# Kernel optimization log

Hardware: AMD Instinct MI355X
Metric: run time of the kernel (lower is better)

The kernel has to match this reference:

```python
import jax, jax.numpy as jnp
import numpy as np

N = 50257      # num nodes / vocab
E = 1_608_224  # num edges (~32 avg degree)
D = 64         # static_feat_dim == embed_dim
OUT = 50257    # output classes
M = 2048       # nodes in batch (node_ids)


def setup_inputs() -> dict:
    key = jax.random.key(0)
    ks = jax.random.split(key, 16)
    w = lambda k, s: jax.random.normal(k, s, jnp.float32) * 0.05
    return dict(
        x=jax.random.normal(ks[0], (N, D), jnp.float32),
        src=jax.random.randint(ks[1], (E,), 0, N, jnp.int32),
        dst=jax.random.randint(ks[2], (E,), 0, N, jnp.int32),
        node_ids=jax.random.randint(ks[3], (M,), 0, N, jnp.int32),
        # GCNConv weights for the three GRU gates
        Wz=w(ks[4], (D, D)), bz=jnp.zeros((D,), jnp.float32),
        Wr=w(ks[5], (D, D)), br=jnp.zeros((D,), jnp.float32),
        Wh=w(ks[6], (D, D)), bh=jnp.zeros((D,), jnp.float32),
        # Linear(2D -> D) gate mixers
        Lz=w(ks[7], (2 * D, D)), lbz=jnp.zeros((D,), jnp.float32),
        Lr=w(ks[8], (2 * D, D)), lbr=jnp.zeros((D,), jnp.float32),
        Lh=w(ks[9], (2 * D, D)), lbh=jnp.zeros((D,), jnp.float32),
        # NodePredictor MLP
        W1=w(ks[10], (D, D)), b1=jnp.zeros((D,), jnp.float32),
        W2=w(ks[11], (D, OUT)), b2=jnp.zeros((OUT,), jnp.float32),
    )


def _gcn(x, src, dst, W, b, enorm, snorm):
    """GCNConv with self-loops: out = D^-1/2 (A+I) D^-1/2 (x W) + b."""
    xw = x @ W  # [N, D]
    agg = jnp.zeros_like(xw).at[dst].add(xw[src] * enorm[:, None])
    return agg + xw * snorm[:, None] + b


def reference(x, src, dst, node_ids, Wz, bz, Wr, br, Wh, bh,
              Lz, lbz, Lr, lbr, Lh, lbh, W1, b1, W2, b2):
    n = x.shape[0]
    # degree with self-loops, symmetric normalization
    deg = jnp.zeros((n,), x.dtype).at[dst].add(jnp.ones((), x.dtype)) + 1.0
    dinv = jax.lax.rsqrt(deg)
    enorm = dinv[src] * dinv[dst]   # per-edge norm
    snorm = dinv * dinv             # self-loop norm

    H = jnp.zeros((n, Wz.shape[1]), x.dtype)  # TGCN initial hidden state
    Z = jax.nn.sigmoid(
        jnp.concatenate([_gcn(x, src, dst, Wz, bz, enorm, snorm), H], 1) @ Lz + lbz)
    R = jax.nn.sigmoid(
        jnp.concatenate([_gcn(x, src, dst, Wr, br, enorm, snorm), H], 1) @ Lr + lbr)
    Ht = jnp.tanh(
        jnp.concatenate([_gcn(x, src, dst, Wh, bh, enorm, snorm), H * R], 1) @ Lh + lbh)
    H = Z * H + (1.0 - Z) * Ht  # [N, D]

    zn = H[node_ids]                          # gather batch nodes [M, D]
    h = jax.nn.relu(zn @ W1 + b1)             # NodePredictor hidden
    return h @ W2 + b2                        # logits [M, OUT]
```

## Files before the change

### kernel.cpp

```cpp
#include <hip/hip_runtime.h>

#define DD 64
#define HBLK 128
#define CAP 128

typedef __attribute__((ext_vector_type(8))) __bf16 bf16x8;
typedef __attribute__((ext_vector_type(4))) float f32x4;
typedef __attribute__((ext_vector_type(4), aligned(4))) float f32x4a;
typedef unsigned short u16;
typedef unsigned int u32;

__device__ __forceinline__ u16 f2bf(float f) {
  union { float f; u32 u; } v; v.f = f;
  u32 r = v.u + 0x7FFFu + ((v.u >> 16) & 1u);
  return (u16)(r >> 16);
}


__global__ __launch_bounds__(256) void k_prep(
    const int* __restrict__ dst, const int* __restrict__ ids,
    const float* __restrict__ Wz, const float* __restrict__ bz,
    const float* __restrict__ Wh, const float* __restrict__ bh,
    const float* __restrict__ Lz, const float* __restrict__ lbz,
    const float* __restrict__ Lh, const float* __restrict__ lbh,
    const float* __restrict__ W2, const float* __restrict__ b2,
    u32* __restrict__ partial, int* __restrict__ slot, int* __restrict__ pcnt,
    float* __restrict__ Wzl, float* __restrict__ bzl,
    float* __restrict__ Whl, float* __restrict__ bhl,
    u16* __restrict__ W2t, float* __restrict__ b2p,
    int E, int N, int M, int OUTC, int NPAD, int NB4) {
  extern __shared__ u32 lds[];
  const int tid = threadIdx.x, bid = blockIdx.x;

  if (bid < HBLK) {
    for (int i = tid; i < NB4; i += 256) lds[i] = 0;
    __syncthreads();
    for (int e = bid * 256 + tid; e < E; e += HBLK * 256) {
      int d = dst[e];
      atomicAdd(&lds[d >> 2], 1u << ((d & 3) * 8));
    }
    __syncthreads();
    u32* po = partial + (size_t)bid * NB4;
    for (int i = tid; i < NB4; i += 256) po[i] = lds[i];
  } else if (bid == 128) {
    for (int i = tid; i < N; i += 256) slot[i] = 0;
    __syncthreads();
    for (int i = tid; i < M; i += 256) slot[ids[i]] = i + 1;
    for (int i = tid; i < M; i += 256) pcnt[i] = 0;
  } else if (bid == 129 || bid == 130) {
    const float* W = (bid == 129) ? Wz : Wh;
    const float* bb = (bid == 129) ? bz : bh;
    const float* L = (bid == 129) ? Lz : Lh;
    const float* lb = (bid == 129) ? lbz : lbh;
    float* Wo = (bid == 129) ? Wzl : Whl;
    float* bo = (bid == 129) ? bzl : bhl;
    for (int idx = tid; idx < DD * DD; idx += 256) {
      int i = idx >> 6, j = idx & 63;
      float acc = 0.f;
      for (int k = 0; k < DD; ++k) acc += W[i * DD + k] * L[k * DD + j];
      Wo[idx] = acc;
    }
    if (tid < DD) {
      float acc = lb[tid];
      for (int k = 0; k < DD; ++k) acc += bb[k] * L[k * DD + tid];
      bo[tid] = acc;
    }
  } else if (bid < 139) {
    int part = bid - 131;
    int chunk = (NPAD + 7) / 8;
    int lo = part * chunk, hi = min(lo + chunk, NPAD);
    for (int i = lo + tid; i < hi; i += 256) b2p[i] = (i < OUTC) ? b2[i] : 0.f;
  } else {
    u16* tile = (u16*)lds;
    const int NT = NPAD / DD;
    for (int tl = bid - 139; tl < NT; tl += 117) {
      int o0 = tl * DD;
      __syncthreads();
#pragma unroll
      for (int i = 0; i < 16; ++i) {
        int idx = i * 256 + tid;
        int k = idx >> 6, o = idx & 63;
        int oc = o0 + o;
        float v = (oc < OUTC) ? W2[(size_t)k * OUTC + oc] : 0.f;
        tile[o * 66 + k] = f2bf(v);
      }
      __syncthreads();
#pragma unroll
      for (int i = 0; i < 16; ++i) {
        int idx = i * 256 + tid;
        int o = idx >> 6, k = idx & 63;
        W2t[(size_t)(o0 + o) * DD + k] = tile[o * 66 + k];
      }
    }
  }
}


__global__ __launch_bounds__(256) void k_mid(
    const u32* __restrict__ partial, const int* __restrict__ slot,
    const int* __restrict__ src, const int* __restrict__ dst,
    float* __restrict__ dinv, int* __restrict__ pcnt, int* __restrict__ esrc,
    int E, int N, int NB4) {
  int gid = blockIdx.x * 256 + threadIdx.x;
  if (gid < N) {
    int word = gid >> 2, sh = (gid & 3) * 8;
    u32 s = 0;
    for (int p = 0; p < HBLK; ++p) s += (partial[(size_t)p * NB4 + word] >> sh) & 0xFFu;
    dinv[gid] = rsqrtf(1.f + (float)s);
  }
  if (gid < E) {
    int d = dst[gid];
    int s = slot[d];
    if (s) {
      int j = s - 1;
      int p = atomicAdd(&pcnt[j], 1);
      if (p < CAP) esrc[j * CAP + p] = src[gid];
    }
  }
}


__global__ __launch_bounds__(256) void k_hidden(
    const int* __restrict__ ids, const int* __restrict__ slot,
    const float* __restrict__ x, const float* __restrict__ dinv,
    const int* __restrict__ pcnt, const int* __restrict__ esrc,
    const float* __restrict__ Wzl, const float* __restrict__ bzl,
    const float* __restrict__ Whl, const float* __restrict__ bhl,
    const float* __restrict__ W1, const float* __restrict__ b1,
    u16* __restrict__ hB, int M) {
  __shared__ float sWz[DD * DD], sWh[DD * DD], sW1[DD * DD];
  for (int i = threadIdx.x; i < DD * DD; i += 256) {
    sWz[i] = Wzl[i]; sWh[i] = Whl[i]; sW1[i] = W1[i];
  }
  __syncthreads();
  int wv = threadIdx.x >> 6, t = threadIdx.x & 63;
  int i = blockIdx.x * 4 + wv;
  if (i >= M) return;
  int n = ids[i];
  int j = slot[n] - 1;
  int c = min(pcnt[j], CAP);
  const int4* el4 = (const int4*)(esrc + j * CAP);
  float agg = 0.f;
  int k = 0;
  for (; k + 8 <= c; k += 8) {
    int4 a = el4[k >> 2], b = el4[(k >> 2) + 1];
    agg += x[(size_t)a.x * DD + t] * dinv[a.x] + x[(size_t)a.y * DD + t] * dinv[a.y]
         + x[(size_t)a.z * DD + t] * dinv[a.z] + x[(size_t)a.w * DD + t] * dinv[a.w]
         + x[(size_t)b.x * DD + t] * dinv[b.x] + x[(size_t)b.y * DD + t] * dinv[b.y]
         + x[(size_t)b.z * DD + t] * dinv[b.z] + x[(size_t)b.w * DD + t] * dinv[b.w];
  }
  for (; k + 4 <= c; k += 4) {
    int4 a = el4[k >> 2];
    agg += x[(size_t)a.x * DD + t] * dinv[a.x] + x[(size_t)a.y * DD + t] * dinv[a.y]
         + x[(size_t)a.z * DD + t] * dinv[a.z] + x[(size_t)a.w * DD + t] * dinv[a.w];
  }
  const int* el = esrc + j * CAP;
  for (; k < c; ++k) { int s0 = el[k]; agg += x[(size_t)s0 * DD + t] * dinv[s0]; }
  float di = dinv[n];
  float av = agg * di + x[(size_t)n * DD + t] * di * di;
  float z = bzl[t], h = bhl[t];
#pragma unroll 8
  for (int q = 0; q < DD; ++q) {
    float a = __shfl(av, q);
    z += a * sWz[q * DD + t];
    h += a * sWh[q * DD + t];
  }
  float Z = 1.f / (1.f + expf(-z));
  float Ht = tanhf(h);
  float hv = (1.f - Z) * Ht;
  float oacc = b1[t];
#pragma unroll 8
  for (int q = 0; q < DD; ++q) oacc += __shfl(hv, q) * sW1[q * DD + t];
  hB[(size_t)i * DD + t] = f2bf(fmaxf(oacc, 0.f));
}


__global__ __launch_bounds__(256) void k_gemm(const u16* __restrict__ hB, const u16* __restrict__ W2t,
                                              const float* __restrict__ b2p, float* __restrict__ out,
                                              int OUTC) {
  __shared__ float sOut[64][260];
  int lane = threadIdx.x & 63;
  int wave = threadIdx.x >> 6;
  int l15 = lane & 15;
  int g = (lane >> 4) & 3;
  long cbase = (long)blockIdx.x * 256;
  int rl = wave * 16 + l15;

  for (int rb = 0; rb < 8; ++rb) {
    int row = blockIdx.y * 512 + rb * 64 + rl;
    const bf16x8* hrow = (const bf16x8*)(hB + (size_t)row * DD);
    bf16x8 b0 = hrow[g], b1 = hrow[4 + g];

#pragma unroll
    for (int half = 0; half < 2; ++half) {
      long c0 = cbase + half * 128;
      f32x4 acc[8];
#pragma unroll
      for (int s = 0; s < 8; ++s) {
        long wcol = c0 + s * 16 + l15;
        const bf16x8* wr = (const bf16x8*)(W2t + (size_t)wcol * DD);
        bf16x8 a0 = wr[g], a1 = wr[4 + g];
        f32x4 a = {0.f, 0.f, 0.f, 0.f};
        a = __builtin_amdgcn_mfma_f32_16x16x32_bf16(a0, b0, a, 0, 0, 0);
        a = __builtin_amdgcn_mfma_f32_16x16x32_bf16(a1, b1, a, 0, 0, 0);
        acc[s] = a;
      }
#pragma unroll
      for (int s = 0; s < 8; ++s) {
        int cl = half * 128 + s * 16 + g * 4;
        float4 bias = *(const float4*)(b2p + cbase + cl);
        sOut[rl][cl + 0] = acc[s][0] + bias.x;
        sOut[rl][cl + 1] = acc[s][1] + bias.y;
        sOut[rl][cl + 2] = acc[s][2] + bias.z;
        sOut[rl][cl + 3] = acc[s][3] + bias.w;
      }
    }
#pragma unroll
    for (int rr = 0; rr < 16; ++rr) {
      int lr = wave * 16 + rr;
      long grow = blockIdx.y * 512 + rb * 64 + lr;
      long col = cbase + lane * 4;
      f32x4a v;
      v[0] = sOut[lr][lane * 4 + 0];
      v[1] = sOut[lr][lane * 4 + 1];
      v[2] = sOut[lr][lane * 4 + 2];
      v[3] = sOut[lr][lane * 4 + 3];
      float* p = out + (size_t)grow * OUTC + col;
      if (col + 3 < OUTC) {
        *(f32x4a*)p = v;
      } else {
#pragma unroll
        for (int r = 0; r < 4; ++r) if (col + r < OUTC) p[r] = v[r];
      }
    }
  }
}


extern "C" void kernel_launch(void* const* d_in, const int* in_sizes, int n_in,
                              void* d_out, int out_size, void* d_ws, size_t ws_size,
                              hipStream_t stream) {
  const float* x   = (const float*)d_in[0];
  const int*   src = (const int*)d_in[1];
  const int*   dst = (const int*)d_in[2];
  const int*   ids = (const int*)d_in[3];
  const float* Wz  = (const float*)d_in[4];
  const float* bz  = (const float*)d_in[5];
  const float* Wh  = (const float*)d_in[8];
  const float* bh  = (const float*)d_in[9];
  const float* Lz  = (const float*)d_in[10];
  const float* lbz = (const float*)d_in[11];
  const float* Lh  = (const float*)d_in[14];
  const float* lbh = (const float*)d_in[15];
  const float* W1  = (const float*)d_in[16];
  const float* b1  = (const float*)d_in[17];
  const float* W2  = (const float*)d_in[18];
  const float* b2  = (const float*)d_in[19];

  const int N    = in_sizes[0] / DD;
  const int E    = in_sizes[1];
  const int M    = in_sizes[3];
  const int OUTC = in_sizes[19];
  const int NPAD = (OUTC + 255) & ~255;
  const int NB4  = (N + 3) / 4;

  char* w = (char*)d_ws;
  auto carve = [&](size_t bytes) {
    void* p = (void*)w;
    w += (bytes + 255) & ~(size_t)255;
    return p;
  };
  u32*   partial = (u32*)carve((size_t)HBLK * NB4 * 4);
  float* dinv = (float*)carve((size_t)N * 4);
  int*   slot = (int*)carve((size_t)N * 4);
  int*   pcnt = (int*)carve((size_t)M * 4);
  int*   esrc = (int*)carve((size_t)M * CAP * 4);
  float* Wzl  = (float*)carve(DD * DD * 4);
  float* bzl  = (float*)carve(DD * 4);
  float* Whl  = (float*)carve(DD * DD * 4);
  float* bhl  = (float*)carve(DD * 4);
  u16*   hB   = (u16*)carve((size_t)M * DD * 2);
  u16*   W2t  = (u16*)carve((size_t)NPAD * DD * 2);
  float* b2p  = (float*)carve((size_t)NPAD * 4);

  unsigned shmem = (unsigned)(NB4 * 4);
  hipLaunchKernelGGL(k_prep, dim3(256), dim3(256), shmem, stream,
                     dst, ids, Wz, bz, Wh, bh, Lz, lbz, Lh, lbh, W2, b2,
                     partial, slot, pcnt, Wzl, bzl, Whl, bhl, W2t, b2p,
                     E, N, M, OUTC, NPAD, NB4);
  hipLaunchKernelGGL(k_mid, dim3((E + 255) / 256), dim3(256), 0, stream,
                     partial, slot, src, dst, dinv, pcnt, esrc, E, N, NB4);
  hipLaunchKernelGGL(k_hidden, dim3((M + 3) / 4), dim3(256), 0, stream,
                     ids, slot, x, dinv, pcnt, esrc, Wzl, bzl, Whl, bhl, W1, b1, hB, M);
  hipLaunchKernelGGL(k_gemm, dim3(NPAD / 256, M / 512), dim3(256), 0, stream,
                     hB, W2t, b2p, (float*)d_out, OUTC);
}
```

Baseline: 208.0 us.

## Rebalance work: persistent GEMM scheduling, wider histogram, vectorized transpose and degree reduce

The output GEMM becomes a fixed 512-block persistent kernel. Each block walks a contiguous range of (column-tile, 64-row) units, which evens out load and keeps the same W2t tile in cache across consecutive units. The degree histogram uses twice as many blocks (256), and k_prep's grid grows to 400 so more blocks share the W2 transpose. The transpose itself now uses float4 loads and packed 32-bit stores. k_mid reduces a whole packed word per thread and writes four dinv values at once, though it now has to read twice as many partial histograms.

```diff
diff --git a/kernel.cpp b/kernel.cpp
--- a/kernel.cpp
+++ b/kernel.cpp
@@ -1,8 +1,9 @@
 #include <hip/hip_runtime.h>
 
 #define DD 64
-#define HBLK 128
+#define HB2 256
 #define CAP 128
+#define GBLK 512
 
 typedef __attribute__((ext_vector_type(8))) __bf16 bf16x8;
 typedef __attribute__((ext_vector_type(4))) float f32x4;
@@ -32,28 +33,28 @@
   extern __shared__ u32 lds[];
   const int tid = threadIdx.x, bid = blockIdx.x;
 
-  if (bid < HBLK) {
+  if (bid < HB2) {
     for (int i = tid; i < NB4; i += 256) lds[i] = 0;
     __syncthreads();
-    for (int e = bid * 256 + tid; e < E; e += HBLK * 256) {
+    for (int e = bid * 256 + tid; e < E; e += HB2 * 256) {
       int d = dst[e];
       atomicAdd(&lds[d >> 2], 1u << ((d & 3) * 8));
     }
     __syncthreads();
     u32* po = partial + (size_t)bid * NB4;
     for (int i = tid; i < NB4; i += 256) po[i] = lds[i];
-  } else if (bid == 128) {
+  } else if (bid == 256) {
     for (int i = tid; i < N; i += 256) slot[i] = 0;
     __syncthreads();
     for (int i = tid; i < M; i += 256) slot[ids[i]] = i + 1;
     for (int i = tid; i < M; i += 256) pcnt[i] = 0;
-  } else if (bid == 129 || bid == 130) {
-    const float* W = (bid == 129) ? Wz : Wh;
-    const float* bb = (bid == 129) ? bz : bh;
-    const float* L = (bid == 129) ? Lz : Lh;
-    const float* lb = (bid == 129) ? lbz : lbh;
-    float* Wo = (bid == 129) ? Wzl : Whl;
-    float* bo = (bid == 129) ? bzl : bhl;
+  } else if (bid == 257 || bid == 258) {
+    const float* W = (bid == 257) ? Wz : Wh;
+    const float* bb = (bid == 257) ? bz : bh;
+    const float* L = (bid == 257) ? Lz : Lh;
+    const float* lb = (bid == 257) ? lbz : lbh;
+    float* Wo = (bid == 257) ? Wzl : Whl;
+    float* bo = (bid == 257) ? bzl : bhl;
     for (int idx = tid; idx < DD * DD; idx += 256) {
       int i = idx >> 6, j = idx & 63;
       float acc = 0.f;
@@ -65,31 +66,39 @@
       for (int k = 0; k < DD; ++k) acc += bb[k] * L[k * DD + tid];
       bo[tid] = acc;
     }
-  } else if (bid < 139) {
-    int part = bid - 131;
+  } else if (bid < 267) {
+    int part = bid - 259;
     int chunk = (NPAD + 7) / 8;
     int lo = part * chunk, hi = min(lo + chunk, NPAD);
     for (int i = lo + tid; i < hi; i += 256) b2p[i] = (i < OUTC) ? b2[i] : 0.f;
   } else {
     u16* tile = (u16*)lds;
     const int NT = NPAD / DD;
-    for (int tl = bid - 139; tl < NT; tl += 117) {
+    for (int tl = bid - 267; tl < NT; tl += 133) {
       int o0 = tl * DD;
       __syncthreads();
 #pragma unroll
-      for (int i = 0; i < 16; ++i) {
-        int idx = i * 256 + tid;
-        int k = idx >> 6, o = idx & 63;
-        int oc = o0 + o;
-        float v = (oc < OUTC) ? W2[(size_t)k * OUTC + oc] : 0.f;
-        tile[o * 66 + k] = f2bf(v);
+      for (int it = 0; it < 4; ++it) {
+        int idx = it * 256 + tid;
+        int k = idx >> 4, ob = (idx & 15) * 4;
+        int oc = o0 + ob;
+        f32x4a v;
+        if (oc + 3 < OUTC) {
+          v = *(const f32x4a*)(W2 + (size_t)k * OUTC + oc);
+        } else {
+#pragma unroll
+          for (int j = 0; j < 4; ++j) v[j] = (oc + j < OUTC) ? W2[(size_t)k * OUTC + oc + j] : 0.f;
+        }
+#pragma unroll
+        for (int j = 0; j < 4; ++j) tile[(ob + j) * 66 + k] = f2bf(v[j]);
       }
       __syncthreads();
 #pragma unroll
-      for (int i = 0; i < 16; ++i) {
-        int idx = i * 256 + tid;
-        int o = idx >> 6, k = idx & 63;
-        W2t[(size_t)(o0 + o) * DD + k] = tile[o * 66 + k];
+      for (int it = 0; it < 8; ++it) {
+        int idx = it * 256 + tid;
+        int o = idx >> 5, kk = (idx & 31) * 2;
+        u32 pk = (u32)tile[o * 66 + kk] | ((u32)tile[o * 66 + kk + 1] << 16);
+        *(u32*)(W2t + (size_t)(o0 + o) * DD + kk) = pk;
       }
     }
   }
@@ -102,11 +111,22 @@
     float* __restrict__ dinv, int* __restrict__ pcnt, int* __restrict__ esrc,
     int E, int N, int NB4) {
   int gid = blockIdx.x * 256 + threadIdx.x;
-  if (gid < N) {
-    int word = gid >> 2, sh = (gid & 3) * 8;
-    u32 s = 0;
-    for (int p = 0; p < HBLK; ++p) s += (partial[(size_t)p * NB4 + word] >> sh) & 0xFFu;
-    dinv[gid] = rsqrtf(1.f + (float)s);
+  if (gid < NB4) {
+    u32 s0 = 0, s1 = 0, s2 = 0, s3 = 0;
+    for (int p = 0; p < HB2; ++p) {
+      u32 w = partial[(size_t)p * NB4 + gid];
+      s0 += w & 0xFFu; s1 += (w >> 8) & 0xFFu; s2 += (w >> 16) & 0xFFu; s3 += (w >> 24) & 0xFFu;
+    }
+    int n = gid * 4;
+    f32x4a dv;
+    dv[0] = rsqrtf(1.f + (float)s0); dv[1] = rsqrtf(1.f + (float)s1);
+    dv[2] = rsqrtf(1.f + (float)s2); dv[3] = rsqrtf(1.f + (float)s3);
+    if (n + 3 < N) {
+      *(f32x4a*)(dinv + n) = dv;
+    } else {
+#pragma unroll
+      for (int j = 0; j < 4; ++j) if (n + j < N) dinv[n + j] = dv[j];
+    }
   }
   if (gid < E) {
     int d = dst[gid];
@@ -177,17 +197,24 @@
 
 __global__ __launch_bounds__(256) void k_gemm(const u16* __restrict__ hB, const u16* __restrict__ W2t,
                                               const float* __restrict__ b2p, float* __restrict__ out,
-                                              int OUTC) {
+                                              int OUTC, int NUNIT, int NYB) {
   __shared__ float sOut[64][260];
   int lane = threadIdx.x & 63;
   int wave = threadIdx.x >> 6;
   int l15 = lane & 15;
   int g = (lane >> 4) & 3;
-  long cbase = (long)blockIdx.x * 256;
   int rl = wave * 16 + l15;
 
-  for (int rb = 0; rb < 8; ++rb) {
-    int row = blockIdx.y * 512 + rb * 64 + rl;
+  int per = NUNIT / GBLK, rem = NUNIT % GBLK;
+  int bid = blockIdx.x;
+  int start = bid * per + min(bid, rem);
+  int cnt = per + (bid < rem);
+
+  for (int u = start; u < start + cnt; ++u) {
+    int xs = u / NYB;
+    int yb = u % NYB;
+    long cbase = (long)xs * 256;
+    int row = yb * 64 + rl;
     const bf16x8* hrow = (const bf16x8*)(hB + (size_t)row * DD);
     bf16x8 b0 = hrow[g], b1 = hrow[4 + g];
 
@@ -218,7 +245,7 @@
 #pragma unroll
     for (int rr = 0; rr < 16; ++rr) {
       int lr = wave * 16 + rr;
-      long grow = blockIdx.y * 512 + rb * 64 + lr;
+      long grow = yb * 64 + lr;
       long col = cbase + lane * 4;
       f32x4a v;
       v[0] = sOut[lr][lane * 4 + 0];
@@ -263,6 +290,8 @@
   const int OUTC = in_sizes[19];
   const int NPAD = (OUTC + 255) & ~255;
   const int NB4  = (N + 3) / 4;
+  const int NYB  = M / 64;
+  const int NUNIT = (NPAD / 256) * NYB;
 
   char* w = (char*)d_ws;
   auto carve = [&](size_t bytes) {
@@ -270,7 +299,7 @@
     w += (bytes + 255) & ~(size_t)255;
     return p;
   };
-  u32*   partial = (u32*)carve((size_t)HBLK * NB4 * 4);
+  u32*   partial = (u32*)carve((size_t)HB2 * NB4 * 4);
   float* dinv = (float*)carve((size_t)N * 4);
   int*   slot = (int*)carve((size_t)N * 4);
   int*   pcnt = (int*)carve((size_t)M * 4);
@@ -284,7 +313,7 @@
   float* b2p  = (float*)carve((size_t)NPAD * 4);
 
   unsigned shmem = (unsigned)(NB4 * 4);
-  hipLaunchKernelGGL(k_prep, dim3(256), dim3(256), shmem, stream,
+  hipLaunchKernelGGL(k_prep, dim3(400), dim3(256), shmem, stream,
                      dst, ids, Wz, bz, Wh, bh, Lz, lbz, Lh, lbh, W2, b2,
                      partial, slot, pcnt, Wzl, bzl, Whl, bhl, W2t, b2p,
                      E, N, M, OUTC, NPAD, NB4);
@@ -292,6 +321,6 @@
                      partial, slot, src, dst, dinv, pcnt, esrc, E, N, NB4);
   hipLaunchKernelGGL(k_hidden, dim3((M + 3) / 4), dim3(256), 0, stream,
                      ids, slot, x, dinv, pcnt, esrc, Wzl, bzl, Whl, bhl, W1, b1, hB, M);
-  hipLaunchKernelGGL(k_gemm, dim3(NPAD / 256, M / 512), dim3(256), 0, stream,
-                     hB, W2t, b2p, (float*)d_out, OUTC);
-}
+  hipLaunchKernelGGL(k_gemm, dim3(GBLK), dim3(256), 0, stream,
+                     hB, W2t, b2p, (float*)d_out, OUTC, NUNIT, NYB);
+}
```

Result: slower. 250.8 us (+20.6%).

## Stage pre-swizzled W2 tile in LDS and shrink output staging buffer

Applied to the files above, without the earlier changes.

The prep kernel now writes W2t in an MFMA-fragment-swizzled layout, so each 256-column slice is a contiguous 32KB block. The GEMM kernel copies its slice into LDS once and then reads fragments with conflict-free lane-indexed loads, instead of re-fetching W2 from global memory for every row block. The output staging buffer is halved and flushed per 128-column half with 2-wide stores. This trades a larger LDS footprint (~66KB vs ~66KB before) and narrower stores for less global traffic on W2.

```diff
diff --git a/kernel.cpp b/kernel.cpp
--- a/kernel.cpp
+++ b/kernel.cpp
@@ -7,6 +7,7 @@
 typedef __attribute__((ext_vector_type(8))) __bf16 bf16x8;
 typedef __attribute__((ext_vector_type(4))) float f32x4;
 typedef __attribute__((ext_vector_type(4), aligned(4))) float f32x4a;
+typedef __attribute__((ext_vector_type(2), aligned(4))) float f32x2a;
 typedef unsigned short u16;
 typedef unsigned int u32;
 
@@ -89,7 +90,13 @@
       for (int i = 0; i < 16; ++i) {
         int idx = i * 256 + tid;
         int o = idx >> 6, k = idx & 63;
-        W2t[(size_t)(o0 + o) * DD + k] = tile[o * 66 + k];
+        int col = o0 + o;
+        int c = col & 255, slice = col >> 8;
+        int half = (c >> 7) & 1, s = (c >> 4) & 7, l15 = c & 15;
+        int a01 = k >> 5, g = (k >> 3) & 3, j = k & 7;
+        size_t didx = (size_t)slice * 16384 +
+                      (size_t)((half * 8 + s) * 128 + a01 * 64 + g * 16 + l15) * 8 + j;
+        W2t[didx] = tile[o * 66 + k];
       }
     }
   }
@@ -178,13 +185,22 @@
 __global__ __launch_bounds__(256) void k_gemm(const u16* __restrict__ hB, const u16* __restrict__ W2t,
                                               const float* __restrict__ b2p, float* __restrict__ out,
                                               int OUTC) {
-  __shared__ float sOut[64][260];
+  __shared__ u16 sW[16384];
+  __shared__ float sOut[64][132];
   int lane = threadIdx.x & 63;
   int wave = threadIdx.x >> 6;
   int l15 = lane & 15;
   int g = (lane >> 4) & 3;
+  int rl = wave * 16 + l15;
   long cbase = (long)blockIdx.x * 256;
-  int rl = wave * 16 + l15;
+
+  {
+    const uint4* gsrc = (const uint4*)(W2t + (size_t)blockIdx.x * 16384);
+    uint4* sdst = (uint4*)sW;
+    for (int i = threadIdx.x; i < 2048; i += 256) sdst[i] = gsrc[i];
+  }
+  __syncthreads();
+  const bf16x8* sWf = (const bf16x8*)sW;
 
   for (int rb = 0; rb < 8; ++rb) {
     int row = blockIdx.y * 512 + rb * 64 + rl;
@@ -197,9 +213,9 @@
       f32x4 acc[8];
 #pragma unroll
       for (int s = 0; s < 8; ++s) {
-        long wcol = c0 + s * 16 + l15;
-        const bf16x8* wr = (const bf16x8*)(W2t + (size_t)wcol * DD);
-        bf16x8 a0 = wr[g], a1 = wr[4 + g];
+        int base16 = (half * 8 + s) * 128;
+        bf16x8 a0 = sWf[base16 + lane];
+        bf16x8 a1 = sWf[base16 + 64 + lane];
         f32x4 a = {0.f, 0.f, 0.f, 0.f};
         a = __builtin_amdgcn_mfma_f32_16x16x32_bf16(a0, b0, a, 0, 0, 0);
         a = __builtin_amdgcn_mfma_f32_16x16x32_bf16(a1, b1, a, 0, 0, 0);
@@ -207,30 +223,29 @@
       }
 #pragma unroll
       for (int s = 0; s < 8; ++s) {
-        int cl = half * 128 + s * 16 + g * 4;
-        float4 bias = *(const float4*)(b2p + cbase + cl);
-        sOut[rl][cl + 0] = acc[s][0] + bias.x;
-        sOut[rl][cl + 1] = acc[s][1] + bias.y;
-        sOut[rl][cl + 2] = acc[s][2] + bias.z;
-        sOut[rl][cl + 3] = acc[s][3] + bias.w;
-      }
-    }
-#pragma unroll
-    for (int rr = 0; rr < 16; ++rr) {
-      int lr = wave * 16 + rr;
-      long grow = blockIdx.y * 512 + rb * 64 + lr;
-      long col = cbase + lane * 4;
-      f32x4a v;
-      v[0] = sOut[lr][lane * 4 + 0];
-      v[1] = sOut[lr][lane * 4 + 1];
-      v[2] = sOut[lr][lane * 4 + 2];
-      v[3] = sOut[lr][lane * 4 + 3];
-      float* p = out + (size_t)grow * OUTC + col;
-      if (col + 3 < OUTC) {
-        *(f32x4a*)p = v;
-      } else {
-#pragma unroll
-        for (int r = 0; r < 4; ++r) if (col + r < OUTC) p[r] = v[r];
+        int cl = s * 16 + g * 4;
+        float4 bias = *(const float4*)(b2p + c0 + cl);
+        f32x4 v;
+        v[0] = acc[s][0] + bias.x;
+        v[1] = acc[s][1] + bias.y;
+        v[2] = acc[s][2] + bias.z;
+        v[3] = acc[s][3] + bias.w;
+        *(f32x4*)(&sOut[rl][cl]) = v;
+      }
+#pragma unroll
+      for (int rr = 0; rr < 16; ++rr) {
+        int lr = wave * 16 + rr;
+        long grow = blockIdx.y * 512 + rb * 64 + lr;
+        long col = c0 + lane * 2;
+        f32x2a v2;
+        v2[0] = sOut[lr][lane * 2];
+        v2[1] = sOut[lr][lane * 2 + 1];
+        float* p = out + (size_t)grow * OUTC + col;
+        if (col + 1 < OUTC) {
+          *(f32x2a*)p = v2;
+        } else if (col < OUTC) {
+          *p = v2[0];
+        }
       }
     }
   }
```

Measured after the change: 202.1 us. 2.9% less time.
